# Performance work log

Measured on AMD Instinct MI355X. Metric: run time of the kernel, lower is better.

## Reference

```python
import jax, jax.numpy as jnp
import numpy as np

D = 128
EMB = 1024
B, S = 4, 4096


def setup_inputs() -> dict:
    key = jax.random.key(0)
    ks = jax.random.split(key, 7)
    scale = 1.0 / np.sqrt(EMB)
    return {
        "X": jax.random.normal(ks[0], (B, S, EMB), dtype=jnp.float32),
        "lam": jnp.float32(0.8),
        "Wq": jax.random.uniform(ks[1], (EMB, 2 * D), jnp.float32, -scale, scale),
        "bq": jax.random.uniform(ks[2], (2 * D,), jnp.float32, -scale, scale),
        "Wk": jax.random.uniform(ks[3], (EMB, 2 * D), jnp.float32, -scale, scale),
        "bk": jax.random.uniform(ks[4], (2 * D,), jnp.float32, -scale, scale),
        "Wv": jax.random.uniform(ks[5], (EMB, D), jnp.float32, -scale, scale),
        "bv": jax.random.uniform(ks[6], (D,), jnp.float32, -scale, scale),
    }


def reference(X, lam, Wq, bq, Wk, bk, Wv, bv):
    # Projections: Q,K are [B,S,2d]; V is [B,S,d]
    Q = X @ Wq + bq
    K = X @ Wk + bk
    V = X @ Wv + bv
    Q1, Q2 = Q[..., :D], Q[..., D:]
    K1, K2 = K[..., :D], K[..., D:]
    s = 1.0 / jnp.sqrt(jnp.float32(D))
    # Dual QK^T scores [B,S,S]
    A1 = jnp.einsum("bqd,bkd->bqk", Q1, K1) * s
    A2 = jnp.einsum("bqd,bkd->bqk", Q2, K2) * s
    P = jax.nn.softmax(A1, axis=-1) - lam * jax.nn.softmax(A2, axis=-1)
    return jnp.einsum("bqk,bkd->bqd", P, V)
```

## Files before the change

### kernel.cpp

```cpp
#include <hip/hip_runtime.h>
#include <hip/hip_bf16.h>


typedef __attribute__((ext_vector_type(8))) short bf16x8;
typedef __attribute__((ext_vector_type(4))) float f32x4;
typedef __attribute__((ext_vector_type(16))) float f32x16;

#define MFMA16(a, b, c) __builtin_amdgcn_mfma_f32_16x16x32_bf16((a), (b), (c), 0, 0, 0)
#define MFMA32(a, b, c) __builtin_amdgcn_mfma_f32_32x32x16_bf16((a), (b), (c), 0, 0, 0)

typedef const __attribute__((address_space(1))) void gas_void;
typedef __attribute__((address_space(3))) void las_void;
#define GLOAD16(G, L) __builtin_amdgcn_global_load_lds((gas_void*)(G), (las_void*)(L), 16, 0, 0)

__device__ __forceinline__ unsigned short f2bf(float x) {
    union { float f; unsigned u; } v; v.f = x;
    return (unsigned short)((v.u + 0x7FFFu + ((v.u >> 16) & 1u)) >> 16);
}
__device__ __forceinline__ unsigned pk2bf(float a, float b) {
    __hip_bfloat162 h = __float22bfloat162_rn(float2{a, b});
    union { __hip_bfloat162 h2; unsigned u; } cv; cv.h2 = h;
    return cv.u;
}
__device__ __forceinline__ float fexp2(float x) {
    float r; asm("v_exp_f32 %0, %1" : "=v"(r) : "v"(x)); return r;
}

__global__ __launch_bounds__(256) void wtrans_kernel(
    const float* __restrict__ Wq, const float* __restrict__ Wk,
    const float* __restrict__ Wv, unsigned short* __restrict__ Wt) {
    int tid = blockIdx.x * 256 + threadIdx.x;
    int k = tid & 1023, n = tid >> 10;
    float v;
    if (n < 256)      v = Wq[k * 256 + n];
    else if (n < 512) v = Wk[k * 256 + (n - 256)];
    else              v = Wv[k * 128 + (n - 512)];
    Wt[tid] = f2bf(v);
}

__global__ __launch_bounds__(256) void proj_kernel(
    const float* __restrict__ X, const unsigned short* __restrict__ Wt,
    const float* __restrict__ bq, const float* __restrict__ bk,
    const float* __restrict__ bv,
    unsigned short* __restrict__ Qs, unsigned short* __restrict__ Kb,
    unsigned short* __restrict__ Vb) {
    __shared__ alignas(16) char lds[16384];
    const int nt = blockIdx.y;
    const int m0 = blockIdx.x * 128;
    const int t = threadIdx.x, w = t >> 6, l = t & 63, c = l & 15, g = l >> 4;
    const int wm = w >> 1, wn = w & 1;
    const unsigned short* Wrow = Wt + (long)(nt * 128) * 1024;

    f32x4 acc[4][4];
    const f32x4 fz = {0.f, 0.f, 0.f, 0.f};
#pragma unroll
    for (int i = 0; i < 4; i++)
#pragma unroll
        for (int j = 0; j < 4; j++) acc[i][j] = fz;

    const int srow = t >> 1, sh = t & 1;
    const int sswz = (srow & 7) << 4;
    for (int k0 = 0; k0 < 1024; k0 += 32) {
        const float* xs = X + (long)(m0 + srow) * 1024 + k0 + sh * 16;
        float4 f0 = *(const float4*)(xs + 0);
        float4 f1 = *(const float4*)(xs + 4);
        float4 f2 = *(const float4*)(xs + 8);
        float4 f3 = *(const float4*)(xs + 12);
        const unsigned short* wsc = Wrow + (long)srow * 1024 + k0 + sh * 16;
        uint4 w0 = *(const uint4*)(wsc + 0);
        uint4 w1 = *(const uint4*)(wsc + 8);
        uint4 xa, xb;
        xa.x = pk2bf(f0.x, f0.y); xa.y = pk2bf(f0.z, f0.w);
        xa.z = pk2bf(f1.x, f1.y); xa.w = pk2bf(f1.z, f1.w);
        xb.x = pk2bf(f2.x, f2.y); xb.y = pk2bf(f2.z, f2.w);
        xb.z = pk2bf(f3.x, f3.y); xb.w = pk2bf(f3.z, f3.w);
        int base = srow * 64 + sh * 32;
        *(uint4*)(lds + ((base + 0) ^ sswz)) = xa;
        *(uint4*)(lds + ((base + 16) ^ sswz)) = xb;
        *(uint4*)(lds + 8192 + ((base + 0) ^ sswz)) = w0;
        *(uint4*)(lds + 8192 + ((base + 16) ^ sswz)) = w1;
        __syncthreads();

        bf16x8 af[4];
#pragma unroll
        for (int am = 0; am < 4; am++) {
            int r_ = wm * 64 + am * 16 + c;
            af[am] = *(const bf16x8*)(lds + ((r_ * 64 + g * 16) ^ ((c & 7) << 4)));
        }
#pragma unroll
        for (int bn = 0; bn < 4; bn++) {
            int r_ = wn * 64 + bn * 16 + c;
            bf16x8 bfr = *(const bf16x8*)(lds + 8192 + ((r_ * 64 + g * 16) ^ ((c & 7) << 4)));
#pragma unroll
            for (int am = 0; am < 4; am++) acc[am][bn] = MFMA16(af[am], bfr, acc[am][bn]);
        }
        __syncthreads();
    }

    const float QSCALE = 0.08838834764831845f * 1.4426950408889634f;
    const float* bias; float scale; unsigned short* outp; int ostride, ocol0, boff;
    if (nt < 2)      { bias = bq; boff = nt * 128;       scale = QSCALE; outp = Qs; ostride = 256; ocol0 = nt * 128; }
    else if (nt < 4) { bias = bk; boff = (nt - 2) * 128; scale = 1.0f;   outp = Kb; ostride = 256; ocol0 = (nt - 2) * 128; }
    else             { bias = bv; boff = 0;              scale = 1.0f;   outp = Vb; ostride = 128; ocol0 = 0; }
#pragma unroll
    for (int bn = 0; bn < 4; bn++) {
        int ncol = wn * 64 + bn * 16 + c;
        float bb = bias[boff + ncol];
#pragma unroll
        for (int am = 0; am < 4; am++) {
#pragma unroll
            for (int r = 0; r < 4; r++) {
                long row = m0 + wm * 64 + am * 16 + 4 * g + r;
                outp[row * ostride + ocol0 + ncol] = f2bf((acc[am][bn][r] + bb) * scale);
            }
        }
    }
}

__global__ __launch_bounds__(256) void vtrans_kernel(
    const unsigned short* __restrict__ Vb, unsigned short* __restrict__ Vt) {
    int tid = blockIdx.x * 256 + threadIdx.x;
    int s = tid & 4095, d = (tid >> 12) & 127, b = tid >> 19;
    Vt[tid] = Vb[(((long)b << 12) + s) * 128 + d];
}

__global__ __launch_bounds__(512) void attn3_kernel(
    const unsigned short* __restrict__ Qs, const unsigned short* __restrict__ Kb,
    const unsigned short* __restrict__ Vt,
    float* __restrict__ Po, float* __restrict__ Ps, int nsplit, int ks) {
    __shared__ alignas(16) char lds[98304];
    const int t = threadIdx.x;
    const int w = t >> 6, l = t & 63, r31 = l & 31, hi = l >> 5;
    const int wq = w >> 1, br = w & 1;

    const int total = gridDim.x;
    const int lin = (blockIdx.x & 7) * (total >> 3) + (blockIdx.x >> 3);
    const int grp = lin >> 5, qb = lin & 31;
    const int b = grp / nsplit, split = grp % nsplit;

    const long qrow = (long)b * 4096 + qb * 128 + wq * 32 + r31;
    bf16x8 qf[8];
    const unsigned short* Qp = Qs + qrow * 256 + br * 128 + hi * 8;
#pragma unroll
    for (int ds = 0; ds < 8; ds++) qf[ds] = *(const bf16x8*)(Qp + ds * 16);

    f32x16 o[4];
    const f32x16 oz = {};
#pragma unroll
    for (int dt = 0; dt < 4; dt++) o[dt] = oz;
    float m = -1e30f, s = 0.f;

    const int krow = w * 4 + (l >> 4);
    const int kc = (l & 15) * 16;
    const int ksrc_rot = (kc - krow * 16) & 255;
    const int vd = w * 16 + (l >> 2);
    const int vc = (l & 3) * 16;
    const long kbb = (long)b * 4096;
    const char* KbB = (const char*)Kb;
    const char* VtB = (const char*)Vt + ((long)b * 128 + vd) * 8192 +
                      ((vc - ((vd >> 1) & 3) * 16) & 63);
    char* dst0 = lds + w * 1024;

    const int kb0 = split * ks, kend = kb0 + ks;
    const int nt = ks >> 5;
#define STAGE(KB_, BUF_)                                                       \
    {                                                                          \
        const char* s1_ = KbB + (kbb + (KB_) + krow) * 512 + ksrc_rot;         \
        char* d_ = dst0 + (BUF_)*24576;                                        \
        GLOAD16(s1_, d_);                                                      \
        GLOAD16(s1_ + 256, d_ + 8192);                                         \
        GLOAD16(VtB + (long)(KB_)*2, d_ + 16384);                              \
    }

    int kro[8];
#pragma unroll
    for (int ds = 0; ds < 8; ds++)
        kro[ds] = br * 8192 + r31 * 256 + ((ds * 32 + hi * 16 + r31 * 16) & 255);
    int vro0[4], vro1[4];
#pragma unroll
    for (int dt = 0; dt < 4; dt++) {
        int vr = dt * 32 + r31, rot = ((vr >> 1) & 3) * 16;
        vro0[dt] = 16384 + vr * 64 + ((hi * 16 + rot) & 63);
        vro1[dt] = 16384 + vr * 64 + ((32 + hi * 16 + rot) & 63);
    }

#define FENCE_TOP(N)                                                           \
    asm volatile("s_waitcnt vmcnt(" #N ")" ::: "memory");                      \
    __builtin_amdgcn_sched_barrier(0);                                         \
    __builtin_amdgcn_s_barrier();                                              \
    __builtin_amdgcn_sched_barrier(0);

#define QKTILE(PN, TI)                                                         \
    {                                                                          \
        const char* kp_ = lds + ((TI) & 3) * 24576;                            \
        f32x16 qa_ = oz, qb_ = oz;                                             \
        _Pragma("unroll") for (int d_ = 0; d_ < 4; d_++) {                     \
            bf16x8 ka_ = *(const bf16x8*)(kp_ + kro[d_]);                      \
            bf16x8 kb_ = *(const bf16x8*)(kp_ + kro[d_ + 4]);                  \
            qa_ = MFMA32(ka_, qf[d_], qa_);                                    \
            qb_ = MFMA32(kb_, qf[d_ + 4], qb_);                                \
        }                                                                      \
        _Pragma("unroll") for (int i_ = 0; i_ < 16; i_++)                      \
            PN[i_] = qa_[i_] + qb_[i_];                                        \
    }

#define SOFTPV(PC, TI)                                                         \
    {                                                                          \
        float x0 = fmaxf(fmaxf(PC[0], PC[1]), fmaxf(PC[2], PC[3]));            \
        float x1 = fmaxf(fmaxf(PC[4], PC[5]), fmaxf(PC[6], PC[7]));            \
        float x2 = fmaxf(fmaxf(PC[8], PC[9]), fmaxf(PC[10], PC[11]));          \
        float x3 = fmaxf(fmaxf(PC[12], PC[13]), fmaxf(PC[14], PC[15]));        \
        float lmx = fmaxf(fmaxf(x0, x1), fmaxf(x2, x3));                       \
        lmx = fmaxf(lmx, __shfl_xor(lmx, 32));                                 \
        if (__any(lmx > m + 8.f)) {                                            \
            float mn = fmaxf(m, lmx);                                          \
            float al = fexp2(m - mn);                                          \
            s *= al; m = mn;                                                   \
            _Pragma("unroll") for (int dt_ = 0; dt_ < 4; dt_++) o[dt_] *= al;  \
        }                                                                      \
        float pe[16];                                                          \
        _Pragma("unroll") for (int i_ = 0; i_ < 16; i_++)                      \
            pe[i_] = fexp2(PC[i_] - m);                                        \
        float s0 = (pe[0] + pe[1]) + (pe[2] + pe[3]);                          \
        float s1 = (pe[4] + pe[5]) + (pe[6] + pe[7]);                          \
        float s2 = (pe[8] + pe[9]) + (pe[10] + pe[11]);                        \
        float s3 = (pe[12] + pe[13]) + (pe[14] + pe[15]);                      \
        float ps_ = (s0 + s1) + (s2 + s3);                                     \
        ps_ += __shfl_xor(ps_, 32);                                            \
        s += ps_;                                                              \
        unsigned cA = pk2bf(pe[0], pe[1]), cB = pk2bf(pe[2], pe[3]);           \
        unsigned cC = pk2bf(pe[4], pe[5]), cD = pk2bf(pe[6], pe[7]);           \
        asm volatile("v_permlane32_swap_b32 %0, %1" : "+v"(cA), "+v"(cC));     \
        asm volatile("v_permlane32_swap_b32 %0, %1" : "+v"(cB), "+v"(cD));     \
        unsigned dA = pk2bf(pe[8], pe[9]), dB = pk2bf(pe[10], pe[11]);         \
        unsigned dC = pk2bf(pe[12], pe[13]), dD = pk2bf(pe[14], pe[15]);       \
        asm volatile("v_permlane32_swap_b32 %0, %1" : "+v"(dA), "+v"(dC));     \
        asm volatile("v_permlane32_swap_b32 %0, %1" : "+v"(dB), "+v"(dD));     \
        union { uint4 u; bf16x8 v; } pb0_, pb1_;                               \
        pb0_.u = uint4{cA, cB, cC, cD};                                        \
        pb1_.u = uint4{dA, dB, dC, dD};                                        \
        const char* vb_ = lds + ((TI) & 3) * 24576;                            \
        _Pragma("unroll") for (int dt_ = 0; dt_ < 4; dt_++) {                  \
            bf16x8 vf0 = *(const bf16x8*)(vb_ + vro0[dt_]);                    \
            bf16x8 vf1 = *(const bf16x8*)(vb_ + vro1[dt_]);                    \
            o[dt_] = MFMA32(vf0, pb0_.v, o[dt_]);                              \
            o[dt_] = MFMA32(vf1, pb1_.v, o[dt_]);                              \
        }                                                                      \
    }

#define STEP(PC, PN, I)                                                        \
    {                                                                          \
        FENCE_TOP(3)                                                           \
        {                                                                      \
            int i3_ = (I) + 3;                                                 \
            int kn_ = (i3_ < nt) ? kb0 + (i3_ << 5) : kb0;                     \
            STAGE(kn_, i3_ & 3);                                               \
        }                                                                      \
        QKTILE(PN, (I) + 1)                                                    \
        SOFTPV(PC, (I))                                                        \
    }

    STAGE(kb0, 0);
    STAGE(kb0 + 32, 1);
    STAGE(kb0 + 64, 2);
    f32x16 pA, pB;
    FENCE_TOP(6)
    QKTILE(pA, 0)

    int it = 0;
    for (; it + 2 < nt; it += 2) {
        STEP(pA, pB, it)
        STEP(pB, pA, it + 1)
    }
    STEP(pA, pB, nt - 2)
    FENCE_TOP(3)
    SOFTPV(pB, nt - 1)
    asm volatile("s_waitcnt vmcnt(0)" ::: "memory");

    float* po = Po + ((qrow * nsplit + split) * 2 + br) * 128;
#pragma unroll
    for (int dt = 0; dt < 4; dt++) {
#pragma unroll
        for (int rg = 0; rg < 4; rg++) {
            float4 v;
            v.x = o[dt][rg * 4 + 0];
            v.y = o[dt][rg * 4 + 1];
            v.z = o[dt][rg * 4 + 2];
            v.w = o[dt][rg * 4 + 3];
            *(float4*)(po + dt * 32 + rg * 8 + hi * 4) = v;
        }
    }
    if (hi == 0)
        *(float2*)(Ps + (qrow * nsplit + split) * 4 + br * 2) = float2{m, s};
#undef STAGE
#undef FENCE_TOP
#undef QKTILE
#undef SOFTPV
#undef STEP
}

__global__ __launch_bounds__(256) void combine_kernel(
    const float* __restrict__ Po, const float* __restrict__ Ps,
    const float* __restrict__ lam_p, float* __restrict__ out, int nsplit) {
    int tid = blockIdx.x * 256 + threadIdx.x;
    int q = tid >> 5, dq = (tid & 31) * 4;
    float M1 = -1e30f, M2 = -1e30f;
    for (int s = 0; s < nsplit; s++) {
        float4 st = *(const float4*)(Ps + (long)(q * nsplit + s) * 4);
        M1 = fmaxf(M1, st.x); M2 = fmaxf(M2, st.z);
    }
    float S1 = 0.f, S2 = 0.f;
    float a0 = 0.f, a1 = 0.f, a2 = 0.f, a3 = 0.f;
    float b0 = 0.f, b1 = 0.f, b2 = 0.f, b3 = 0.f;
    for (int s = 0; s < nsplit; s++) {
        float4 st = *(const float4*)(Ps + (long)(q * nsplit + s) * 4);
        float w1 = fexp2(st.x - M1), w2 = fexp2(st.z - M2);
        S1 += st.y * w1; S2 += st.w * w2;
        const float* p1 = Po + (((long)q * nsplit + s) * 2 + 0) * 128 + dq;
        const float* p2 = Po + (((long)q * nsplit + s) * 2 + 1) * 128 + dq;
        float4 v1 = *(const float4*)p1;
        float4 v2 = *(const float4*)p2;
        a0 += v1.x * w1; a1 += v1.y * w1; a2 += v1.z * w1; a3 += v1.w * w1;
        b0 += v2.x * w2; b1 += v2.y * w2; b2 += v2.z * w2; b3 += v2.w * w2;
    }
    float lam = *lam_p;
    float i1 = 1.f / S1, i2 = lam / S2;
    float4 v;
    v.x = a0 * i1 - b0 * i2;
    v.y = a1 * i1 - b1 * i2;
    v.z = a2 * i1 - b2 * i2;
    v.w = a3 * i1 - b3 * i2;
    *(float4*)(out + (long)q * 128 + dq) = v;
}

extern "C" void kernel_launch(void* const* d_in, const int* in_sizes, int n_in,
                              void* d_out, int out_size, void* d_ws, size_t ws_size,
                              hipStream_t stream) {
    const float* X   = (const float*)d_in[0];
    const float* lam = (const float*)d_in[1];
    const float* Wq  = (const float*)d_in[2];
    const float* bq  = (const float*)d_in[3];
    const float* Wk  = (const float*)d_in[4];
    const float* bk  = (const float*)d_in[5];
    const float* Wv  = (const float*)d_in[6];
    const float* bv  = (const float*)d_in[7];
    char* ws = (char*)d_ws;
    unsigned short* Qs = (unsigned short*)(ws);
    unsigned short* Kb = (unsigned short*)(ws + (8u << 20));
    unsigned short* Vb = (unsigned short*)(ws + (16u << 20));
    unsigned short* Vt = (unsigned short*)(ws + (20u << 20));
    unsigned short* Wt = (unsigned short*)(ws + (24u << 20));
    const size_t base = (size_t)26 << 20;
    const size_t NQ = 16384;
    int nsplit = 1;
    if (ws_size >= base + NQ * 4 * 2 * 128 * 4 + NQ * 4 * 4 * 4)      nsplit = 4;
    else if (ws_size >= base + NQ * 2 * 2 * 128 * 4 + NQ * 2 * 4 * 4) nsplit = 2;
    float* Po = (float*)(ws + base);
    float* Ps = (float*)(ws + base + NQ * (size_t)nsplit * 2 * 128 * 4);

    wtrans_kernel<<<2560, 256, 0, stream>>>(Wq, Wk, Wv, Wt);
    proj_kernel<<<dim3(128, 5), 256, 0, stream>>>(X, Wt, bq, bk, bv, Qs, Kb, Vb);
    vtrans_kernel<<<8192, 256, 0, stream>>>(Vb, Vt);
    attn3_kernel<<<128 * nsplit, 512, 0, stream>>>(Qs, Kb, Vt, Po, Ps,
                                                   nsplit, 4096 / nsplit);
    combine_kernel<<<2048, 256, 0, stream>>>(Po, Ps, lam, (float*)d_out, nsplit);
}
```

Baseline: 171.0 us.

## Software-pipeline attention into QK, PV and softmax stages; tile the V transpose

The attention kernel now runs a three-stage software pipeline: each step issues the QK MFMAs for the next tile and the PV MFMAs for the previous tile under raised wave priority, then does softmax on the current tile. The LDS ring grows from four to five buffers so the extra tile in flight stays resident. This aims to hide softmax latency behind matrix work, at the cost of more registers and LDS, and launch_bounds now asks for two blocks per CU. The V transpose kernel is also rewritten to stage 64x64 tiles through shared memory with 16-byte loads and stores instead of scattered 2-byte accesses.

```diff
diff --git a/kernel.cpp b/kernel.cpp
--- a/kernel.cpp
+++ b/kernel.cpp
@@ -119,16 +119,35 @@
 
 __global__ __launch_bounds__(256) void vtrans_kernel(
     const unsigned short* __restrict__ Vb, unsigned short* __restrict__ Vt) {
-    int tid = blockIdx.x * 256 + threadIdx.x;
-    int s = tid & 4095, d = (tid >> 12) & 127, b = tid >> 19;
-    Vt[tid] = Vb[(((long)b << 12) + s) * 128 + d];
-}
-
-__global__ __launch_bounds__(512) void attn3_kernel(
+    __shared__ unsigned short lds[64][72];
+    const int bid = blockIdx.x;
+    const int db = bid & 1, sb = (bid >> 1) & 63, b = bid >> 7;
+    const int s0 = sb * 64, d0 = db * 64;
+    const int t = threadIdx.x;
+    const int r = t >> 2, c4 = t & 3;
+    const unsigned short* src = Vb + ((long)(b * 4096 + s0 + r)) * 128 + d0;
+    uint4 u0 = *(const uint4*)(src + c4 * 8);
+    uint4 u1 = *(const uint4*)(src + (c4 + 4) * 8);
+    *(uint4*)(&lds[r][c4 * 8]) = u0;
+    *(uint4*)(&lds[r][(c4 + 4) * 8]) = u1;
+    __syncthreads();
+    const int dd = t >> 2;
+    unsigned short* dst = Vt + ((long)(b * 128 + d0 + dd)) * 4096 + s0;
+#pragma unroll
+    for (int cc2 = 0; cc2 < 2; cc2++) {
+        int cc = c4 + cc2 * 4;
+        unsigned short tmp[8];
+#pragma unroll
+        for (int j = 0; j < 8; j++) tmp[j] = lds[cc * 8 + j][dd];
+        *(uint4*)(dst + cc * 8) = *(const uint4*)tmp;
+    }
+}
+
+__global__ __launch_bounds__(512, 2) void attn4_kernel(
     const unsigned short* __restrict__ Qs, const unsigned short* __restrict__ Kb,
     const unsigned short* __restrict__ Vt,
     float* __restrict__ Po, float* __restrict__ Ps, int nsplit, int ks) {
-    __shared__ alignas(16) char lds[98304];
+    __shared__ alignas(16) char lds[122880];
     const int t = threadIdx.x;
     const int w = t >> 6, l = t & 63, r31 = l & 31, hi = l >> 5;
     const int wq = w >> 1, br = w & 1;
@@ -161,7 +180,7 @@
                       ((vc - ((vd >> 1) & 3) * 16) & 63);
     char* dst0 = lds + w * 1024;
 
-    const int kb0 = split * ks, kend = kb0 + ks;
+    const int kb0 = split * ks;
     const int nt = ks >> 5;
 #define STAGE(KB_, BUF_)                                                       \
     {                                                                          \
@@ -184,32 +203,37 @@
         vro1[dt] = 16384 + vr * 64 + ((32 + hi * 16 + rot) & 63);
     }
 
-#define FENCE_TOP(N)                                                           \
-    asm volatile("s_waitcnt vmcnt(" #N ")" ::: "memory");                      \
-    __builtin_amdgcn_sched_barrier(0);                                         \
-    __builtin_amdgcn_s_barrier();                                              \
-    __builtin_amdgcn_sched_barrier(0);
-
-#define QKTILE(PN, TI)                                                         \
-    {                                                                          \
-        const char* kp_ = lds + ((TI) & 3) * 24576;                            \
-        f32x16 qa_ = oz, qb_ = oz;                                             \
+#define QKTILE(QA_, QB_, BI_)                                                  \
+    {                                                                          \
+        const char* kp_ = lds + (BI_)*24576;                                   \
         _Pragma("unroll") for (int d_ = 0; d_ < 4; d_++) {                     \
             bf16x8 ka_ = *(const bf16x8*)(kp_ + kro[d_]);                      \
-            bf16x8 kb_ = *(const bf16x8*)(kp_ + kro[d_ + 4]);                  \
-            qa_ = MFMA32(ka_, qf[d_], qa_);                                    \
-            qb_ = MFMA32(kb_, qf[d_ + 4], qb_);                                \
+            bf16x8 kb2_ = *(const bf16x8*)(kp_ + kro[d_ + 4]);                 \
+            QA_ = MFMA32(ka_, qf[d_], QA_);                                    \
+            QB_ = MFMA32(kb2_, qf[d_ + 4], QB_);                               \
         }                                                                      \
-        _Pragma("unroll") for (int i_ = 0; i_ < 16; i_++)                      \
-            PN[i_] = qa_[i_] + qb_[i_];                                        \
-    }
-
-#define SOFTPV(PC, TI)                                                         \
-    {                                                                          \
-        float x0 = fmaxf(fmaxf(PC[0], PC[1]), fmaxf(PC[2], PC[3]));            \
-        float x1 = fmaxf(fmaxf(PC[4], PC[5]), fmaxf(PC[6], PC[7]));            \
-        float x2 = fmaxf(fmaxf(PC[8], PC[9]), fmaxf(PC[10], PC[11]));          \
-        float x3 = fmaxf(fmaxf(PC[12], PC[13]), fmaxf(PC[14], PC[15]));        \
+    }
+
+#define PVTILE(PK0_, PK1_, BI_)                                                \
+    {                                                                          \
+        const char* vb_ = lds + (BI_)*24576;                                   \
+        union { uint4 u; bf16x8 v; } u0_, u1_;                                 \
+        u0_.u = PK0_; u1_.u = PK1_;                                            \
+        _Pragma("unroll") for (int dt_ = 0; dt_ < 4; dt_++) {                  \
+            bf16x8 vf0 = *(const bf16x8*)(vb_ + vro0[dt_]);                    \
+            bf16x8 vf1 = *(const bf16x8*)(vb_ + vro1[dt_]);                    \
+            o[dt_] = MFMA32(vf0, u0_.v, o[dt_]);                               \
+            o[dt_] = MFMA32(vf1, u1_.v, o[dt_]);                               \
+        }                                                                      \
+    }
+
+#define SOFTMAX(QC0, QC1, PD0, PD1)                                            \
+    {                                                                          \
+        _Pragma("unroll") for (int i_ = 0; i_ < 16; i_++) QC0[i_] += QC1[i_];  \
+        float x0 = fmaxf(fmaxf(QC0[0], QC0[1]), fmaxf(QC0[2], QC0[3]));        \
+        float x1 = fmaxf(fmaxf(QC0[4], QC0[5]), fmaxf(QC0[6], QC0[7]));        \
+        float x2 = fmaxf(fmaxf(QC0[8], QC0[9]), fmaxf(QC0[10], QC0[11]));      \
+        float x3 = fmaxf(fmaxf(QC0[12], QC0[13]), fmaxf(QC0[14], QC0[15]));    \
         float lmx = fmaxf(fmaxf(x0, x1), fmaxf(x2, x3));                       \
         lmx = fmaxf(lmx, __shfl_xor(lmx, 32));                                 \
         if (__any(lmx > m + 8.f)) {                                            \
@@ -220,12 +244,12 @@
         }                                                                      \
         float pe[16];                                                          \
         _Pragma("unroll") for (int i_ = 0; i_ < 16; i_++)                      \
-            pe[i_] = fexp2(PC[i_] - m);                                        \
-        float s0 = (pe[0] + pe[1]) + (pe[2] + pe[3]);                          \
-        float s1 = (pe[4] + pe[5]) + (pe[6] + pe[7]);                          \
-        float s2 = (pe[8] + pe[9]) + (pe[10] + pe[11]);                        \
-        float s3 = (pe[12] + pe[13]) + (pe[14] + pe[15]);                      \
-        float ps_ = (s0 + s1) + (s2 + s3);                                     \
+            pe[i_] = fexp2(QC0[i_] - m);                                       \
+        float s0_ = (pe[0] + pe[1]) + (pe[2] + pe[3]);                         \
+        float s1_ = (pe[4] + pe[5]) + (pe[6] + pe[7]);                         \
+        float s2_ = (pe[8] + pe[9]) + (pe[10] + pe[11]);                       \
+        float s3_ = (pe[12] + pe[13]) + (pe[14] + pe[15]);                     \
+        float ps_ = (s0_ + s1_) + (s2_ + s3_);                                 \
         ps_ += __shfl_xor(ps_, 32);                                            \
         s += ps_;                                                              \
         unsigned cA = pk2bf(pe[0], pe[1]), cB = pk2bf(pe[2], pe[3]);           \
@@ -236,45 +260,46 @@
         unsigned dC = pk2bf(pe[12], pe[13]), dD = pk2bf(pe[14], pe[15]);       \
         asm volatile("v_permlane32_swap_b32 %0, %1" : "+v"(dA), "+v"(dC));     \
         asm volatile("v_permlane32_swap_b32 %0, %1" : "+v"(dB), "+v"(dD));     \
-        union { uint4 u; bf16x8 v; } pb0_, pb1_;                               \
-        pb0_.u = uint4{cA, cB, cC, cD};                                        \
-        pb1_.u = uint4{dA, dB, dC, dD};                                        \
-        const char* vb_ = lds + ((TI) & 3) * 24576;                            \
-        _Pragma("unroll") for (int dt_ = 0; dt_ < 4; dt_++) {                  \
-            bf16x8 vf0 = *(const bf16x8*)(vb_ + vro0[dt_]);                    \
-            bf16x8 vf1 = *(const bf16x8*)(vb_ + vro1[dt_]);                    \
-            o[dt_] = MFMA32(vf0, pb0_.v, o[dt_]);                              \
-            o[dt_] = MFMA32(vf1, pb1_.v, o[dt_]);                              \
+        PD0 = uint4{cA, cB, cC, cD};                                           \
+        PD1 = uint4{dA, dB, dC, dD};                                           \
+    }
+
+#define BODY(QC0, QC1, QN0, QN1, PU0, PU1, PD0, PD1, I_)                       \
+    {                                                                          \
+        asm volatile("s_waitcnt vmcnt(3)" ::: "memory");                       \
+        __builtin_amdgcn_sched_barrier(0);                                     \
+        __builtin_amdgcn_s_barrier();                                          \
+        __builtin_amdgcn_sched_barrier(0);                                     \
+        {                                                                      \
+            int i3_ = (I_) + 3;                                                \
+            int kn_ = (i3_ < nt) ? kb0 + (i3_ << 5) : kb0;                     \
+            STAGE(kn_, i3_ % 5);                                               \
         }                                                                      \
-    }
-
-#define STEP(PC, PN, I)                                                        \
-    {                                                                          \
-        FENCE_TOP(3)                                                           \
-        {                                                                      \
-            int i3_ = (I) + 3;                                                 \
-            int kn_ = (i3_ < nt) ? kb0 + (i3_ << 5) : kb0;                     \
-            STAGE(kn_, i3_ & 3);                                               \
-        }                                                                      \
-        QKTILE(PN, (I) + 1)                                                    \
-        SOFTPV(PC, (I))                                                        \
+        QN0 = oz; QN1 = oz;                                                    \
+        __builtin_amdgcn_s_setprio(1);                                         \
+        if ((I_) + 1 < nt) QKTILE(QN0, QN1, ((I_) + 1) % 5)                    \
+        if ((I_) > 0) PVTILE(PU0, PU1, ((I_) + 4) % 5)                         \
+        __builtin_amdgcn_s_setprio(0);                                         \
+        SOFTMAX(QC0, QC1, PD0, PD1)                                            \
     }
 
     STAGE(kb0, 0);
     STAGE(kb0 + 32, 1);
     STAGE(kb0 + 64, 2);
-    f32x16 pA, pB;
-    FENCE_TOP(6)
-    QKTILE(pA, 0)
-
-    int it = 0;
-    for (; it + 2 < nt; it += 2) {
-        STEP(pA, pB, it)
-        STEP(pB, pA, it + 1)
-    }
-    STEP(pA, pB, nt - 2)
-    FENCE_TOP(3)
-    SOFTPV(pB, nt - 1)
+    asm volatile("s_waitcnt vmcnt(6)" ::: "memory");
+    __builtin_amdgcn_sched_barrier(0);
+    __builtin_amdgcn_s_barrier();
+    __builtin_amdgcn_sched_barrier(0);
+    f32x16 qaA = oz, qbA = oz, qaB = oz, qbB = oz;
+    QKTILE(qaA, qbA, 0)
+    uint4 pkA0 = {0, 0, 0, 0}, pkA1 = {0, 0, 0, 0};
+    uint4 pkB0 = {0, 0, 0, 0}, pkB1 = {0, 0, 0, 0};
+
+    for (int it = 0; it < nt; it += 2) {
+        BODY(qaA, qbA, qaB, qbB, pkB0, pkB1, pkA0, pkA1, it)
+        BODY(qaB, qbB, qaA, qbA, pkA0, pkA1, pkB0, pkB1, it + 1)
+    }
+    PVTILE(pkB0, pkB1, (nt + 4) % 5)
     asm volatile("s_waitcnt vmcnt(0)" ::: "memory");
 
     float* po = Po + ((qrow * nsplit + split) * 2 + br) * 128;
@@ -293,10 +318,10 @@
     if (hi == 0)
         *(float2*)(Ps + (qrow * nsplit + split) * 4 + br * 2) = float2{m, s};
 #undef STAGE
-#undef FENCE_TOP
 #undef QKTILE
-#undef SOFTPV
-#undef STEP
+#undef PVTILE
+#undef SOFTMAX
+#undef BODY
 }
 
 __global__ __launch_bounds__(256) void combine_kernel(
@@ -360,8 +385,8 @@
 
     wtrans_kernel<<<2560, 256, 0, stream>>>(Wq, Wk, Wv, Wt);
     proj_kernel<<<dim3(128, 5), 256, 0, stream>>>(X, Wt, bq, bk, bv, Qs, Kb, Vb);
-    vtrans_kernel<<<8192, 256, 0, stream>>>(Vb, Vt);
-    attn3_kernel<<<128 * nsplit, 512, 0, stream>>>(Qs, Kb, Vt, Po, Ps,
+    vtrans_kernel<<<512, 256, 0, stream>>>(Vb, Vt);
+    attn4_kernel<<<128 * nsplit, 512, 0, stream>>>(Qs, Kb, Vt, Po, Ps,
                                                    nsplit, 4096 / nsplit);
     combine_kernel<<<2048, 256, 0, stream>>>(Po, Ps, lam, (float*)d_out, nsplit);
 }
```

After: 172.1 us. About the same (+0.7%).
